# Performance work log

Measured on AMD Instinct MI355X. Metric: run time of the kernel, lower is better.

The kernel has to match this reference:

```python
import jax, jax.numpy as jnp
import numpy as np

D_MODEL = 1024
EXPAND = 2
D_INNER = EXPAND * D_MODEL  # 2048
D_STATE = 16
D_CONV = 4
DT_RANK = D_INNER  # non-int dt_rank resolves to d_inner
BATCH, SEQ = 2, 1024
EPS = 1e-5


def setup_inputs() -> dict:
    key = jax.random.key(0)
    ks = jax.random.split(key, 9)
    s = 0.02
    return {
        "x": jax.random.normal(ks[0], (BATCH, SEQ, D_MODEL), jnp.float32),
        "rms_w": jnp.ones((D_MODEL,), jnp.float32),
        "W_in": jax.random.normal(ks[1], (D_MODEL, 2 * D_INNER), jnp.float32) * s,
        "conv_w": jax.random.normal(ks[2], (D_INNER, 1, D_CONV), jnp.float32) * 0.2,
        "conv_b": jax.random.normal(ks[3], (D_INNER,), jnp.float32) * 0.02,
        "W_x": jax.random.normal(ks[4], (D_INNER, DT_RANK + 2 * D_STATE), jnp.float32) * s,
        "W_dt": jax.random.normal(ks[5], (DT_RANK, D_INNER), jnp.float32) * s,
        "A_log": jax.random.normal(ks[6], (D_INNER, D_STATE), jnp.float32),
        "W_out": jax.random.normal(ks[7], (D_INNER, D_MODEL), jnp.float32) * s,
    }


def _rmsnorm(x, w):
    var = jnp.mean(jnp.square(x), axis=-1, keepdims=True)
    return x * jax.lax.rsqrt(var + EPS) * w


def _forward(x, rms_w, W_in, conv_w, conv_b, W_x, W_dt, A_log, W_out):
    B, L, _ = x.shape
    residual = x
    xn = _rmsnorm(x, rms_w)
    xr = xn @ W_in                                  # [B,L,2*d_inner]
    xs, res = jnp.split(xr, 2, axis=-1)
    # causal depthwise conv1d: torch pads d_conv-1 both sides then slices [:L]
    xc = jnp.transpose(xs, (0, 2, 1))               # [B,d_inner,L]
    xc = jnp.pad(xc, ((0, 0), (0, 0), (D_CONV - 1, 0)))
    xc = jax.lax.conv_general_dilated(
        xc, conv_w, window_strides=(1,), padding='VALID',
        dimension_numbers=('NCH', 'OIH', 'NCH'), feature_group_count=D_INNER)
    xc = xc + conv_b[None, :, None]
    xs = jax.nn.silu(jnp.transpose(xc, (0, 2, 1)))  # [B,L,d_inner]
    x_ssm = xs @ W_x                                # [B,L,d_inner+2*d_state]
    dt, Bm, Cm = jnp.split(x_ssm, [D_INNER, D_INNER + D_STATE], axis=-1)
    dt = jax.nn.softplus(dt @ W_dt)                 # [B,L,d_inner]
    A = -jnp.exp(A_log)                             # [d_inner,d_state]
    A_disc = jnp.exp(A[None, None] * dt[..., None])            # [B,L,d_inner,N]
    Bx = dt[..., None] * Bm[:, :, None, :] * xs[..., None]     # [B,L,d_inner,N]

    def step(h, inp):
        Ad_t, Bx_t, C_t = inp                       # [B,d_inner,N],[B,d_inner,N],[B,N]
        h = Ad_t * h + Bx_t
        y = jnp.einsum('bdn,bn->bd', h, C_t)
        return h, y

    h0 = jnp.zeros((B, D_INNER, D_STATE), xs.dtype)
    _, ys = jax.lax.scan(
        step, h0,
        (jnp.transpose(A_disc, (1, 0, 2, 3)),
         jnp.transpose(Bx, (1, 0, 2, 3)),
         jnp.transpose(Cm, (1, 0, 2))))
    y = jnp.transpose(ys, (1, 0, 2))                # [B,L,d_inner]
    y = y * jax.nn.silu(res)
    out = y @ W_out
    return residual + out


def reference(x, rms_w, W_in, conv_w, conv_b, W_x, W_dt, A_log, W_out):
    return _forward(x, rms_w, W_in, conv_w, conv_b, W_x, W_dt, A_log, W_out)
```

## Files before the change

kernel.cpp:

```cpp
#include <hip/hip_runtime.h>
#include <math.h>

#define B_SZ   2
#define LSEQ   1024
#define DMODEL 1024
#define DINNER 2048
#define DSTATE 16
#define NTOK   (B_SZ * LSEQ)
#define NSSM   (DINNER + 2 * DSTATE)
#define CL     32
#define NCH    (LSEQ / CL)
#define NC     (B_SZ * DINNER)

typedef unsigned short ushort;
typedef __attribute__((ext_vector_type(8))) ushort ushort8;
typedef __attribute__((ext_vector_type(8))) __bf16 bf16x8;
typedef __attribute__((ext_vector_type(4))) float floatx4;

__device__ __forceinline__ float softplus_f(float x) {
  return (x > 20.f) ? x : __logf(1.f + __expf(x));
}
__device__ __forceinline__ float silu_f(float x) {
  return x / (1.f + __expf(-x));
}
__device__ __forceinline__ float bf2f(ushort u) {
  return __uint_as_float(((unsigned)u) << 16);
}
__device__ __forceinline__ ushort f2bf(float f) {
  unsigned u = __float_as_uint(f);
  return (ushort)((u + 0x7FFFu + ((u >> 16) & 1u)) >> 16);
}

__global__ __launch_bounds__(256) void rmsnorm_kernel(
    const float* __restrict__ x, const float* __restrict__ w,
    ushort* __restrict__ xn) {
  int row = blockIdx.x;
  const float* xrow = x + (size_t)row * DMODEL;
  float v[4];
  float ss = 0.f;
#pragma unroll
  for (int i = 0; i < 4; i++) {
    v[i] = xrow[threadIdx.x + 256 * i];
    ss += v[i] * v[i];
  }
  __shared__ float wsum[4];
  int lane = threadIdx.x & 63, wid = threadIdx.x >> 6;
#pragma unroll
  for (int off = 1; off < 64; off <<= 1) ss += __shfl_xor(ss, off);
  if (lane == 0) wsum[wid] = ss;
  __syncthreads();
  float tot = wsum[0] + wsum[1] + wsum[2] + wsum[3];
  float scale = rsqrtf(tot / (float)DMODEL + 1e-5f);
#pragma unroll
  for (int i = 0; i < 4; i++) {
    int j = threadIdx.x + 256 * i;
    xn[(size_t)row * DMODEL + j] = f2bf(v[i] * scale * w[j]);
  }
}

__global__ __launch_bounds__(256) void transpose_w(
    const float* __restrict__ W, ushort* __restrict__ Wt, int K, int N) {
  __shared__ float tile[64][65];
  int n0 = blockIdx.x * 64, k0 = blockIdx.y * 64;
  int c = threadIdx.x & 63, rb = (threadIdx.x >> 6) << 4;
#pragma unroll
  for (int i = 0; i < 16; i++) {
    int k = k0 + rb + i;
    if (k < K && n0 + c < N) tile[rb + i][c] = W[(size_t)k * N + n0 + c];
  }
  __syncthreads();
#pragma unroll
  for (int i = 0; i < 16; i++) {
    int n = n0 + rb + i;
    if (n < N && k0 + c < K)
      Wt[(size_t)n * K + k0 + c] = f2bf(tile[c][rb + i]);
  }
}

__global__ __launch_bounds__(256) void gemm_mfma(
    const ushort* __restrict__ A, int lda,
    const ushort* __restrict__ Bt, int ldb,
    int N, int K, int mode,
    void* __restrict__ C0, void* __restrict__ C1,
    const float* __restrict__ addend) {
  __shared__ ushort As[128][32];
  __shared__ ushort Bs[128][32];
  const int bm = blockIdx.y * 128, bn = blockIdx.x * 128;
  const int tid = threadIdx.x;
  const int wave = tid >> 6, lane = tid & 63;
  const int srow = tid >> 2;
  const int scol = (tid & 3) << 3;
  const int wm = (wave & 1) << 6, wn = (wave >> 1) << 6;
  const int lrow = lane & 15, quad = lane >> 4;

  const int brow0 = min(bn + srow, N - 1);
  const int brow1 = min(bn + srow + 64, N - 1);
  const ushort* ga0 = A + (size_t)(bm + srow) * lda + scol;
  const ushort* ga1 = A + (size_t)(bm + srow + 64) * lda + scol;
  const ushort* gb0 = Bt + (size_t)brow0 * ldb + scol;
  const ushort* gb1 = Bt + (size_t)brow1 * ldb + scol;

  floatx4 acc[4][4];
#pragma unroll
  for (int i = 0; i < 4; i++)
#pragma unroll
    for (int j = 0; j < 4; j++) acc[i][j] = (floatx4){0.f, 0.f, 0.f, 0.f};

  ushort8 ar0 = *(const ushort8*)ga0, ar1 = *(const ushort8*)ga1;
  ushort8 br0 = *(const ushort8*)gb0, br1 = *(const ushort8*)gb1;
  const int nk = K >> 5;
  for (int kt = 0; kt < nk; kt++) {
    __syncthreads();
    *(ushort8*)&As[srow][scol] = ar0;
    *(ushort8*)&As[srow + 64][scol] = ar1;
    *(ushort8*)&Bs[srow][scol] = br0;
    *(ushort8*)&Bs[srow + 64][scol] = br1;
    __syncthreads();
    if (kt + 1 < nk) {
      int off = (kt + 1) << 5;
      ar0 = *(const ushort8*)(ga0 + off);
      ar1 = *(const ushort8*)(ga1 + off);
      br0 = *(const ushort8*)(gb0 + off);
      br1 = *(const ushort8*)(gb1 + off);
    }
    bf16x8 af[4], bfr[4];
#pragma unroll
    for (int i = 0; i < 4; i++)
      af[i] = __builtin_bit_cast(bf16x8,
          *(const ushort8*)&As[wm + i * 16 + lrow][quad << 3]);
#pragma unroll
    for (int j = 0; j < 4; j++)
      bfr[j] = __builtin_bit_cast(bf16x8,
          *(const ushort8*)&Bs[wn + j * 16 + lrow][quad << 3]);
#pragma unroll
    for (int i = 0; i < 4; i++)
#pragma unroll
      for (int j = 0; j < 4; j++)
        acc[i][j] = __builtin_amdgcn_mfma_f32_16x16x32_bf16(
            af[i], bfr[j], acc[i][j], 0, 0, 0);
  }
  const int m0 = bm + wm, n0 = bn + wn, rq = quad << 2;
#pragma unroll
  for (int i = 0; i < 4; i++) {
#pragma unroll
    for (int j = 0; j < 4; j++) {
#pragma unroll
      for (int r = 0; r < 4; r++) {
        int m = m0 + i * 16 + rq + r;
        int n = n0 + j * 16 + lrow;
        if (n >= N) continue;
        float v = acc[i][j][r];
        if (mode == 0) {
          ((float*)C0)[(size_t)m * N + n] = v + addend[(size_t)m * N + n];
        } else if (mode == 1) {
          if (n < DINNER)
            ((ushort*)C0)[(size_t)m * DINNER + n] = f2bf(v);
          else
            ((ushort*)C1)[(size_t)m * DINNER + n - DINNER] = f2bf(silu_f(v));
        } else if (mode == 2) {
          ((ushort*)C0)[(size_t)m * NSSM + n] = f2bf(v);
          if (n >= DINNER)
            ((float*)C1)[(size_t)m * 32 + n - DINNER] = v;
        } else {
          ((float*)C0)[(size_t)m * DINNER + n] = softplus_f(v);
        }
      }
    }
  }
}

__global__ __launch_bounds__(256) void conv_silu_kernel(
    const ushort* __restrict__ xsraw, const float* __restrict__ cw,
    const float* __restrict__ cb, ushort* __restrict__ xs) {
  int gid = blockIdx.x * 256 + threadIdx.x;
  int c = gid & (DINNER - 1);
  int t = gid >> 11;
  int l = t & (LSEQ - 1);
  float w0 = cw[c * 4 + 0], w1 = cw[c * 4 + 1], w2 = cw[c * 4 + 2], w3 = cw[c * 4 + 3];
  const ushort* col = xsraw + (size_t)t * DINNER + c;
  float acc = cb[c] + w3 * bf2f(col[0]);
  if (l >= 1) acc += w2 * bf2f(col[-DINNER]);
  if (l >= 2) acc += w1 * bf2f(col[-2 * DINNER]);
  if (l >= 3) acc += w0 * bf2f(col[-3 * DINNER]);
  xs[gid] = f2bf(silu_f(acc));
}

__global__ __launch_bounds__(256) void scan_chunk1(
    const float* __restrict__ dt, const ushort* __restrict__ xs,
    const float* __restrict__ bc, const float* __restrict__ A_log,
    float* __restrict__ Bc, float* __restrict__ S) {
  int blk = blockIdx.x;
  int b = blk >> 8;
  int rem = blk & 255;
  int ch = rem >> 3;
  int dblk = rem & 7;
  int d = dblk * 256 + threadIdx.x;
  int c = b * DINNER + d;
  float a[DSTATE];
#pragma unroll
  for (int i = 0; i < 4; i++) {
    float4 v = *(const float4*)(A_log + (size_t)d * DSTATE + 4 * i);
    a[4 * i + 0] = -__expf(v.x);
    a[4 * i + 1] = -__expf(v.y);
    a[4 * i + 2] = -__expf(v.z);
    a[4 * i + 3] = -__expf(v.w);
  }
  float h[DSTATE] = {};
  float Ssum = 0.f;
  size_t t = (size_t)b * LSEQ + (size_t)ch * CL;
#pragma unroll 2
  for (int l = 0; l < CL; l++, t++) {
    float dtv = dt[t * DINNER + d];
    float dx = dtv * bf2f(xs[t * DINNER + d]);
    const float4* Bp = (const float4*)(bc + t * 32);
    float4 b0 = Bp[0], b1 = Bp[1], b2 = Bp[2], b3 = Bp[3];
    float bb[DSTATE] = {b0.x, b0.y, b0.z, b0.w, b1.x, b1.y, b1.z, b1.w,
                        b2.x, b2.y, b2.z, b2.w, b3.x, b3.y, b3.z, b3.w};
#pragma unroll
    for (int n = 0; n < DSTATE; n++)
      h[n] = __expf(a[n] * dtv) * h[n] + dx * bb[n];
    Ssum += dtv;
  }
  float4* outp = (float4*)(Bc + ((size_t)c * NCH + ch) * DSTATE);
  outp[0] = make_float4(h[0], h[1], h[2], h[3]);
  outp[1] = make_float4(h[4], h[5], h[6], h[7]);
  outp[2] = make_float4(h[8], h[9], h[10], h[11]);
  outp[3] = make_float4(h[12], h[13], h[14], h[15]);
  S[c * NCH + ch] = Ssum;
}

__global__ __launch_bounds__(256) void scan_combine(
    const float* __restrict__ A_log, const float* __restrict__ S,
    float* BcHin) {
  int gid = blockIdx.x * 256 + threadIdx.x;
  int c = gid >> 4, n = gid & 15;
  int d = c & (DINNER - 1);
  float a = -__expf(A_log[d * DSTATE + n]);
  float h = 0.f;
  size_t base = (size_t)c * (NCH * DSTATE) + n;
  for (int ch = 0; ch < NCH; ch++) {
    float bcv = BcHin[base + (size_t)ch * DSTATE];
    float decay = __expf(a * S[c * NCH + ch]);
    BcHin[base + (size_t)ch * DSTATE] = h;
    h = decay * h + bcv;
  }
}

__global__ __launch_bounds__(256) void scan_chunk2(
    const float* __restrict__ dt, const ushort* __restrict__ xs,
    const float* __restrict__ bc, const ushort* __restrict__ gate,
    const float* __restrict__ A_log, const float* __restrict__ hin,
    ushort* __restrict__ y) {
  int blk = blockIdx.x;
  int b = blk >> 8;
  int rem = blk & 255;
  int ch = rem >> 3;
  int dblk = rem & 7;
  int d = dblk * 256 + threadIdx.x;
  int c = b * DINNER + d;
  float a[DSTATE];
#pragma unroll
  for (int i = 0; i < 4; i++) {
    float4 v = *(const float4*)(A_log + (size_t)d * DSTATE + 4 * i);
    a[4 * i + 0] = -__expf(v.x);
    a[4 * i + 1] = -__expf(v.y);
    a[4 * i + 2] = -__expf(v.z);
    a[4 * i + 3] = -__expf(v.w);
  }
  float h[DSTATE];
  const float4* hi = (const float4*)(hin + ((size_t)c * NCH + ch) * DSTATE);
#pragma unroll
  for (int i = 0; i < 4; i++) {
    float4 v = hi[i];
    h[4 * i + 0] = v.x; h[4 * i + 1] = v.y; h[4 * i + 2] = v.z; h[4 * i + 3] = v.w;
  }
  size_t t = (size_t)b * LSEQ + (size_t)ch * CL;
#pragma unroll 2
  for (int l = 0; l < CL; l++, t++) {
    float dtv = dt[t * DINNER + d];
    float dx = dtv * bf2f(xs[t * DINNER + d]);
    const float4* Bp = (const float4*)(bc + t * 32);
    const float4* Cp = (const float4*)(bc + t * 32 + 16);
    float4 b0 = Bp[0], b1 = Bp[1], b2 = Bp[2], b3 = Bp[3];
    float4 c0 = Cp[0], c1 = Cp[1], c2 = Cp[2], c3 = Cp[3];
    float bb[DSTATE] = {b0.x, b0.y, b0.z, b0.w, b1.x, b1.y, b1.z, b1.w,
                        b2.x, b2.y, b2.z, b2.w, b3.x, b3.y, b3.z, b3.w};
    float cc[DSTATE] = {c0.x, c0.y, c0.z, c0.w, c1.x, c1.y, c1.z, c1.w,
                        c2.x, c2.y, c2.z, c2.w, c3.x, c3.y, c3.z, c3.w};
    float ysum = 0.f;
#pragma unroll
    for (int n = 0; n < DSTATE; n++) {
      h[n] = __expf(a[n] * dtv) * h[n] + dx * bb[n];
      ysum = fmaf(h[n], cc[n], ysum);
    }
    y[t * DINNER + d] = f2bf(ysum * bf2f(gate[t * DINNER + d]));
  }
}

extern "C" void kernel_launch(void* const* d_in, const int* in_sizes, int n_in,
                              void* d_out, int out_size, void* d_ws, size_t ws_size,
                              hipStream_t stream) {
  const float* x      = (const float*)d_in[0];
  const float* rms_w  = (const float*)d_in[1];
  const float* W_in   = (const float*)d_in[2];
  const float* conv_w = (const float*)d_in[3];
  const float* conv_b = (const float*)d_in[4];
  const float* W_x    = (const float*)d_in[5];
  const float* W_dt   = (const float*)d_in[6];
  const float* A_log  = (const float*)d_in[7];
  const float* W_out  = (const float*)d_in[8];
  float* out = (float*)d_out;

  char* w = (char*)d_ws;
  ushort* xnb   = (ushort*)(w + 0);
  ushort* xsraw = (ushort*)(w + 4194304);
  ushort* gate  = (ushort*)(w + 12582912);
  ushort* xsb   = (ushort*)(w + 20971520);
  ushort* ssmb  = (ushort*)(w + 29360128);
  float*  dtb   = (float*)(w + 37879808);
  ushort* yb    = (ushort*)(w + 54657024);
  ushort* WinT  = (ushort*)(w + 63045632);
  ushort* WxT   = (ushort*)(w + 71434240);
  ushort* WdtT  = (ushort*)(w + 79953920);
  ushort* WoutT = (ushort*)(w + 88342528);
  float* bc = (float*)(w + 0);
  float* S  = (float*)(w + 262144);
  float* Bc = (float*)(w + 4194304);

  transpose_w<<<dim3(64, 16), 256, 0, stream>>>(W_in, WinT, DMODEL, 4096);
  transpose_w<<<dim3(33, 32), 256, 0, stream>>>(W_x, WxT, DINNER, NSSM);
  transpose_w<<<dim3(32, 32), 256, 0, stream>>>(W_dt, WdtT, DINNER, DINNER);
  transpose_w<<<dim3(16, 32), 256, 0, stream>>>(W_out, WoutT, DINNER, DMODEL);

  rmsnorm_kernel<<<NTOK, 256, 0, stream>>>(x, rms_w, xnb);
  gemm_mfma<<<dim3(32, 16), 256, 0, stream>>>(
      xnb, DMODEL, WinT, DMODEL, 4096, DMODEL, 1, xsraw, gate, nullptr);
  conv_silu_kernel<<<(NTOK * DINNER) / 256, 256, 0, stream>>>(xsraw, conv_w, conv_b, xsb);
  gemm_mfma<<<dim3(17, 16), 256, 0, stream>>>(
      xsb, DINNER, WxT, DINNER, NSSM, DINNER, 2, ssmb, bc, nullptr);
  gemm_mfma<<<dim3(16, 16), 256, 0, stream>>>(
      ssmb, NSSM, WdtT, DINNER, DINNER, DINNER, 3, dtb, nullptr, nullptr);
  scan_chunk1<<<B_SZ * NCH * 8, 256, 0, stream>>>(dtb, xsb, bc, A_log, Bc, S);
  scan_combine<<<(NC * DSTATE) / 256, 256, 0, stream>>>(A_log, S, Bc);
  scan_chunk2<<<B_SZ * NCH * 8, 256, 0, stream>>>(dtb, xsb, bc, gate, A_log, Bc, yb);
  gemm_mfma<<<dim3(8, 16), 256, 0, stream>>>(
      yb, DINNER, WoutT, DINNER, DMODEL, DINNER, 0, out, nullptr, x);
}
```

Measured before the change: 390.2 us.

## Double-buffer GEMM LDS tiles and XOR-swizzle to cut bank conflicts

The MFMA GEMM's shared-memory tiles become two ping-pong buffers, which removes one of the two barriers per k-iteration. An XOR swizzle on the 16-byte column chunk is applied to both the stores and the fragment reads, to spread LDS bank accesses. This doubles LDS use per block, which may lower occupancy slightly.

```diff
diff --git a/kernel.cpp b/kernel.cpp
--- a/kernel.cpp
+++ b/kernel.cpp
@@ -83,22 +83,24 @@
     int N, int K, int mode,
     void* __restrict__ C0, void* __restrict__ C1,
     const float* __restrict__ addend) {
-  __shared__ ushort As[128][32];
-  __shared__ ushort Bs[128][32];
+  __shared__ ushort As[2 * 128 * 32];
+  __shared__ ushort Bs[2 * 128 * 32];
   const int bm = blockIdx.y * 128, bn = blockIdx.x * 128;
   const int tid = threadIdx.x;
   const int wave = tid >> 6, lane = tid & 63;
-  const int srow = tid >> 2;
-  const int scol = (tid & 3) << 3;
   const int wm = (wave & 1) << 6, wn = (wave >> 1) << 6;
   const int lrow = lane & 15, quad = lane >> 4;
 
-  const int brow0 = min(bn + srow, N - 1);
-  const int brow1 = min(bn + srow + 64, N - 1);
-  const ushort* ga0 = A + (size_t)(bm + srow) * lda + scol;
-  const ushort* ga1 = A + (size_t)(bm + srow + 64) * lda + scol;
-  const ushort* gb0 = Bt + (size_t)brow0 * ldb + scol;
-  const ushort* gb1 = Bt + (size_t)brow1 * ldb + scol;
+  const int sr = tid >> 2;
+  const int q  = tid & 3;
+  const int swr = (sr ^ (sr >> 2)) & 3;
+  const int pq = (q ^ swr) << 3;
+  const int br0 = min(bn + sr, N - 1);
+  const int br1 = min(bn + sr + 64, N - 1);
+  const ushort* ga0 = A + (size_t)(bm + sr) * lda + (q << 3);
+  const ushort* ga1 = A + (size_t)(bm + sr + 64) * lda + (q << 3);
+  const ushort* gb0 = Bt + (size_t)br0 * ldb + (q << 3);
+  const ushort* gb1 = Bt + (size_t)br1 * ldb + (q << 3);
 
   floatx4 acc[4][4];
 #pragma unroll
@@ -106,32 +108,35 @@
 #pragma unroll
     for (int j = 0; j < 4; j++) acc[i][j] = (floatx4){0.f, 0.f, 0.f, 0.f};
 
-  ushort8 ar0 = *(const ushort8*)ga0, ar1 = *(const ushort8*)ga1;
-  ushort8 br0 = *(const ushort8*)gb0, br1 = *(const ushort8*)gb1;
+  const int swf = ((lrow ^ (lrow >> 2)) & 3);
+  const int fq = ((quad ^ swf) << 3);
+
   const int nk = K >> 5;
+  ushort8 ra0 = *(const ushort8*)ga0, ra1 = *(const ushort8*)ga1;
+  ushort8 rb0 = *(const ushort8*)gb0, rb1 = *(const ushort8*)gb1;
   for (int kt = 0; kt < nk; kt++) {
-    __syncthreads();
-    *(ushort8*)&As[srow][scol] = ar0;
-    *(ushort8*)&As[srow + 64][scol] = ar1;
-    *(ushort8*)&Bs[srow][scol] = br0;
-    *(ushort8*)&Bs[srow + 64][scol] = br1;
+    const int bo = (kt & 1) << 12;
+    *(ushort8*)&As[bo + sr * 32 + pq] = ra0;
+    *(ushort8*)&As[bo + (sr + 64) * 32 + pq] = ra1;
+    *(ushort8*)&Bs[bo + sr * 32 + pq] = rb0;
+    *(ushort8*)&Bs[bo + (sr + 64) * 32 + pq] = rb1;
     __syncthreads();
     if (kt + 1 < nk) {
-      int off = (kt + 1) << 5;
-      ar0 = *(const ushort8*)(ga0 + off);
-      ar1 = *(const ushort8*)(ga1 + off);
-      br0 = *(const ushort8*)(gb0 + off);
-      br1 = *(const ushort8*)(gb1 + off);
+      const int ko = (kt + 1) << 5;
+      ra0 = *(const ushort8*)(ga0 + ko);
+      ra1 = *(const ushort8*)(ga1 + ko);
+      rb0 = *(const ushort8*)(gb0 + ko);
+      rb1 = *(const ushort8*)(gb1 + ko);
     }
     bf16x8 af[4], bfr[4];
 #pragma unroll
     for (int i = 0; i < 4; i++)
       af[i] = __builtin_bit_cast(bf16x8,
-          *(const ushort8*)&As[wm + i * 16 + lrow][quad << 3]);
+          *(const ushort8*)&As[bo + (wm + i * 16 + lrow) * 32 + fq]);
 #pragma unroll
     for (int j = 0; j < 4; j++)
       bfr[j] = __builtin_bit_cast(bf16x8,
-          *(const ushort8*)&Bs[wn + j * 16 + lrow][quad << 3]);
+          *(const ushort8*)&Bs[bo + (wn + j * 16 + lrow) * 32 + fq]);
 #pragma unroll
     for (int i = 0; i < 4; i++)
 #pragma unroll
```

After: 384.9 us. No clear change (-1.4%).
